# Performance work log

Hardware: AMD Instinct MI355X
Metric: run time of the kernel (lower is better)

Reference implementation:

```python
import jax, jax.numpy as jnp
import numpy as np

N_ANCHORS = 8388608  # many images' SSD anchors concatenated
N_CLASSES = 3
GAMMA = 2.0  # focal exponent (alpha=0.9 is defined but unused in the original)


def setup_inputs() -> dict:
    key = jax.random.key(0)
    k1, k2 = jax.random.split(key)
    pred = jax.random.normal(k1, (N_ANCHORS, N_CLASSES), dtype=jnp.float32)
    targ = jax.random.randint(k2, (N_ANCHORS,), 0, 5, dtype=jnp.int64)
    return {"pred": pred, "targ": targ}


def reference(pred, targ):
    # One-hot target: class id 1 -> column 0, class id 3 -> column 1, else column 2
    col = jnp.where(targ == 1, 0, jnp.where(targ == 3, 1, 2))
    t = jax.nn.one_hot(col, N_CLASSES, dtype=pred.dtype)  # [A, 3]

    # Focal-style weight from DETACHED raw logits (faithful: original uses x.detach(),
    # no sigmoid, and w = [1,1,1])
    p = jax.lax.stop_gradient(pred)
    pt = p * t + (1.0 - p) * (1.0 - t)
    weight = (1.0 - pt) ** GAMMA

    # binary_cross_entropy_with_logits with per-element weight, mean reduction
    # stable form: max(x,0) - x*t + log(1 + exp(-|x|))
    bce = jnp.maximum(pred, 0.0) - pred * t + jnp.log1p(jnp.exp(-jnp.abs(pred)))
    return jnp.mean(weight * bce)
```

## Files before the change

### kernel.cpp

```cpp
#include <hip/hip_runtime.h>
#include <math.h>


#define GRID   8192
#define BLOCK  256
#define FBLOCK 1024

typedef float f32x4 __attribute__((ext_vector_type(4)));
typedef int   i32x4 __attribute__((ext_vector_type(4)));

__device__ __forceinline__ float elem_loss(float x, bool is_t) {
    float l   = __logf(1.0f + __expf(-fabsf(x)));
    float bce = fmaxf(x, 0.0f) + l - (is_t ? x : 0.0f);
    float m   = is_t ? (1.0f - x) : x;
    return m * m * bce;
}

__device__ __forceinline__ float group_loss(f32x4 f0, f32x4 f1, f32x4 f2, i32x4 tg) {
    float f[12] = {f0.x, f0.y, f0.z, f0.w,
                   f1.x, f1.y, f1.z, f1.w,
                   f2.x, f2.y, f2.z, f2.w};
    int   tt[4] = {tg.x, tg.y, tg.z, tg.w};
    float acc = 0.0f;
    #pragma unroll
    for (int a = 0; a < 4; ++a) {
        int col = (tt[a] == 1) ? 0 : ((tt[a] == 3) ? 1 : 2);
        #pragma unroll
        for (int j = 0; j < 3; ++j)
            acc += elem_loss(f[a * 3 + j], j == col);
    }
    return acc;
}

__global__ __launch_bounds__(BLOCK) void focal_partial(
        const float* __restrict__ pred,
        const int*   __restrict__ targ,
        float*       __restrict__ partial,
        int n_anchors) {
    const int tid      = blockIdx.x * BLOCK + threadIdx.x;
    const int nthreads = GRID * BLOCK;
    const int groups   = n_anchors >> 2;

    const f32x4* __restrict__ p4 = (const f32x4*)pred;
    const i32x4* __restrict__ t4 = (const i32x4*)targ;

    float acc = 0.0f;

    for (int g = tid; g < groups; g += nthreads) {
        f32x4 f0 = p4[3 * g + 0];
        f32x4 f1 = p4[3 * g + 1];
        f32x4 f2 = p4[3 * g + 2];
        i32x4 tg = t4[g];
        acc += group_loss(f0, f1, f2, tg);
    }
    for (int i = (groups << 2) + tid; i < n_anchors; i += nthreads) {
        int tv  = targ[i];
        int col = (tv == 1) ? 0 : ((tv == 3) ? 1 : 2);
        #pragma unroll
        for (int j = 0; j < 3; ++j)
            acc += elem_loss(pred[i * 3 + j], j == col);
    }

    #pragma unroll
    for (int off = 32; off; off >>= 1)
        acc += __shfl_down(acc, off, 64);

    __shared__ float sm[4];
    const int lane = threadIdx.x & 63;
    const int wave = threadIdx.x >> 6;
    if (lane == 0) sm[wave] = acc;
    __syncthreads();

    if (threadIdx.x == 0)
        partial[blockIdx.x] = sm[0] + sm[1] + sm[2] + sm[3];
}

__global__ __launch_bounds__(FBLOCK) void final_reduce(
        const float* __restrict__ partial, int nparts,
        float* __restrict__ out, float inv_total) {
    const f32x4* __restrict__ p4 = (const f32x4*)partial;
    float acc = 0.0f;
    for (int i = threadIdx.x; 4 * i < nparts; i += FBLOCK) {
        f32x4 v = p4[i];
        acc += (v.x + v.y) + (v.z + v.w);
    }

    #pragma unroll
    for (int off = 32; off; off >>= 1)
        acc += __shfl_down(acc, off, 64);

    __shared__ float sm[FBLOCK / 64];
    const int lane = threadIdx.x & 63;
    const int wave = threadIdx.x >> 6;
    if (lane == 0) sm[wave] = acc;
    __syncthreads();

    if (threadIdx.x == 0) {
        float s = 0.0f;
        #pragma unroll
        for (int w = 0; w < FBLOCK / 64; ++w) s += sm[w];
        out[0] = s * inv_total;
    }
}

extern "C" void kernel_launch(void* const* d_in, const int* in_sizes, int n_in,
                              void* d_out, int out_size, void* d_ws, size_t ws_size,
                              hipStream_t stream) {
    const float* pred = (const float*)d_in[0];
    const int*   targ = (const int*)d_in[1];
    float*       out  = (float*)d_out;
    float*       partial = (float*)d_ws;

    const int n_anchors = in_sizes[1];
    const float inv_total = 1.0f / (3.0f * (float)n_anchors);

    focal_partial<<<GRID, BLOCK, 0, stream>>>(pred, targ, partial, n_anchors);
    final_reduce<<<1, FBLOCK, 0, stream>>>(partial, GRID, out, inv_total);
}
```

Baseline: 28.32 us.

## Coalesce prediction loads and transpose through LDS per block

```diff
diff --git a/kernel.cpp b/kernel.cpp
--- a/kernel.cpp
+++ b/kernel.cpp
@@ -5,6 +5,8 @@
 #define GRID   8192
 #define BLOCK  256
 #define FBLOCK 1024
+#define GPB    256
+#define LDS_STRIDE 13
 
 typedef float f32x4 __attribute__((ext_vector_type(4)));
 typedef int   i32x4 __attribute__((ext_vector_type(4)));
@@ -16,11 +18,8 @@
     return m * m * bce;
 }
 
-__device__ __forceinline__ float group_loss(f32x4 f0, f32x4 f1, f32x4 f2, i32x4 tg) {
-    float f[12] = {f0.x, f0.y, f0.z, f0.w,
-                   f1.x, f1.y, f1.z, f1.w,
-                   f2.x, f2.y, f2.z, f2.w};
-    int   tt[4] = {tg.x, tg.y, tg.z, tg.w};
+__device__ __forceinline__ float group_loss12(const float* f, i32x4 tg) {
+    int tt[4] = {tg.x, tg.y, tg.z, tg.w};
     float acc = 0.0f;
     #pragma unroll
     for (int a = 0; a < 4; ++a) {
@@ -37,23 +36,66 @@
         const int*   __restrict__ targ,
         float*       __restrict__ partial,
         int n_anchors) {
-    const int tid      = blockIdx.x * BLOCK + threadIdx.x;
-    const int nthreads = GRID * BLOCK;
-    const int groups   = n_anchors >> 2;
+    __shared__ float lds[LDS_STRIDE * GPB];
+
+    const int t            = threadIdx.x;
+    const int groups_total = n_anchors >> 2;
+    const int main_groups  = GRID * GPB;
 
     const f32x4* __restrict__ p4 = (const f32x4*)pred;
     const i32x4* __restrict__ t4 = (const i32x4*)targ;
 
     float acc = 0.0f;
 
-    for (int g = tid; g < groups; g += nthreads) {
+    const int gbase = blockIdx.x * GPB;
+    if (gbase + GPB <= groups_total) {
+        const int pbase = blockIdx.x * (3 * GPB);
+        f32x4 s0 = p4[pbase + t];
+        f32x4 s1 = p4[pbase + 256 + t];
+        f32x4 s2 = p4[pbase + 512 + t];
+        i32x4 tg = t4[gbase + t];
+
+        #pragma unroll
+        for (int k = 0; k < 3; ++k) {
+            const int u = 256 * k + t;
+            const int q = u / 3;
+            const int r = u - 3 * q;
+            float* dst = &lds[LDS_STRIDE * q + 4 * r];
+            f32x4 v = (k == 0) ? s0 : ((k == 1) ? s1 : s2);
+            dst[0] = v.x; dst[1] = v.y; dst[2] = v.z; dst[3] = v.w;
+        }
+        __syncthreads();
+
+        float f[12];
+        #pragma unroll
+        for (int j = 0; j < 12; ++j)
+            f[j] = lds[LDS_STRIDE * t + j];
+        acc += group_loss12(f, tg);
+    } else {
+        for (int g = gbase + t; g < groups_total; g += BLOCK) {
+            f32x4 f0 = p4[3 * g + 0];
+            f32x4 f1 = p4[3 * g + 1];
+            f32x4 f2 = p4[3 * g + 2];
+            i32x4 tg = t4[g];
+            float f[12] = {f0.x, f0.y, f0.z, f0.w,
+                           f1.x, f1.y, f1.z, f1.w,
+                           f2.x, f2.y, f2.z, f2.w};
+            acc += group_loss12(f, tg);
+        }
+    }
+
+    const int gtid = blockIdx.x * BLOCK + t;
+    for (int g = main_groups + gtid; g < groups_total; g += GRID * BLOCK) {
         f32x4 f0 = p4[3 * g + 0];
         f32x4 f1 = p4[3 * g + 1];
         f32x4 f2 = p4[3 * g + 2];
         i32x4 tg = t4[g];
-        acc += group_loss(f0, f1, f2, tg);
+        float f[12] = {f0.x, f0.y, f0.z, f0.w,
+                       f1.x, f1.y, f1.z, f1.w,
+                       f2.x, f2.y, f2.z, f2.w};
+        acc += group_loss12(f, tg);
     }
-    for (int i = (groups << 2) + tid; i < n_anchors; i += nthreads) {
+    for (int i = (groups_total << 2) + gtid; i < n_anchors; i += GRID * BLOCK) {
         int tv  = targ[i];
         int col = (tv == 1) ? 0 : ((tv == 3) ? 1 : 2);
         #pragma unroll
@@ -66,12 +108,12 @@
         acc += __shfl_down(acc, off, 64);
 
     __shared__ float sm[4];
-    const int lane = threadIdx.x & 63;
-    const int wave = threadIdx.x >> 6;
+    const int lane = t & 63;
+    const int wave = t >> 6;
     if (lane == 0) sm[wave] = acc;
     __syncthreads();
 
-    if (threadIdx.x == 0)
+    if (t == 0)
         partial[blockIdx.x] = sm[0] + sm[1] + sm[2] + sm[3];
 }
 
```

New measurement: 28.71 us. No clear change (+1.4%).
